# Kernel tuning notes

Measured on AMD Instinct MI355X. Metric: run time of the kernel, lower is better.

Reference implementation:

```python
import jax, jax.numpy as jnp
import numpy as np

B, S, IN, OUT = 4, 2048, 4096, 1024
ROUNDS = 12  # prime_factors(4096) == [2]*12
QMIN, QMAX = -128, 127


def _create_noise(key, shape, lo, hi):
    # Obfuscation noise spanning the data range; exactly corrected in forward.
    return jax.random.uniform(key, shape, jnp.float32, -0.5, 0.5) * (hi - lo)


def setup_inputs() -> dict:
    key = jax.random.key(0)
    ks = jax.random.split(key, 6)
    x = jax.random.normal(ks[0], (B, S, IN), jnp.float32)
    weight = jax.random.normal(ks[1], (OUT, IN), jnp.float32) * 0.02
    bias = jax.random.normal(ks[2], (OUT,), jnp.float32) * 0.02
    weight_noise = _create_noise(ks[3], (OUT, IN), weight.min(), weight.max())
    noise_x = _create_noise(ks[4], (B, S, IN), x.min(), x.max())
    # one random permutation of in_features per round
    perms = jnp.stack([jax.random.permutation(jax.random.fold_in(key, 1000 + r), IN)
                       for r in range(ROUNDS)]).astype(jnp.int32)
    # 2048 random orthogonal 2x2 blocks per round (rotations, like ortho_group with dim=2)
    theta = jax.random.uniform(ks[5], (ROUNDS, IN // 2), jnp.float32, 0.0, 2.0 * np.pi)
    c, s = jnp.cos(theta), jnp.sin(theta)
    row0 = jnp.stack([c, -s], axis=-1)
    row1 = jnp.stack([s, c], axis=-1)
    matrices = jnp.stack([row0, row1], axis=-2)  # (ROUNDS, IN//2, 2, 2)
    return {"x": x, "weight": weight, "bias": bias, "weight_noise": weight_noise,
            "noise_x": noise_x, "permutations": perms, "matrices": matrices}


def _permute_matrix_operation(X, perms, mats):
    # X: (..., n, cols). Each round: gather rows by permutation, then apply a
    # block-diagonal orthogonal transform (G blocks of size f along the n axis).
    lead = X.shape[:-2]
    n, cols = X.shape[-2], X.shape[-1]
    G, f = mats.shape[1], mats.shape[2]
    for r in range(mats.shape[0]):
        X = jnp.take(X, perms[r], axis=-2)
        Xb = X.reshape(lead + (G, f, cols))
        X = jnp.einsum('gij,...gjc->...gic', mats[r], Xb).reshape(lead + (n, cols))
    return X


def _quant_dequant(t):
    # Asymmetric per-tensor quantize -> round -> clamp -> dequantize (int8-style).
    lo, hi = t.min(), t.max()
    scale = (hi - lo) / (QMAX - QMIN)
    zp = jnp.round(QMIN - lo / scale)
    q = jnp.clip(jnp.round(t / scale + zp), QMIN, QMAX)
    return (q - zp) * scale


def reference(x, weight, bias, weight_noise, noise_x, permutations, matrices):
    # inverse-transpose blocks; equals `matrices` for orthogonal blocks, kept explicit for fidelity
    inv_mats_mT = jnp.swapaxes(jnp.linalg.inv(matrices), -1, -2)
    w_plus = weight + weight_noise                                   # (OUT, IN)
    permuted_w = jnp.swapaxes(
        _permute_matrix_operation(jnp.swapaxes(w_plus, -1, -2), permutations, inv_mats_mT), -1, -2)
    qw = _quant_dequant(permuted_w)                                  # (OUT, IN)
    permuted_x = jnp.swapaxes(
        _permute_matrix_operation(jnp.swapaxes(x + noise_x, -1, -2), permutations, matrices), -1, -2)
    qx = _quant_dequant(permuted_x)                                  # (B, S, IN)
    res = qx @ qw.T + bias                                           # quantized matmul + bias
    res = res - x @ weight_noise.T                                   # correction term 1
    res = res - noise_x @ w_plus.T                                   # correction term 2
    return res
```

## Files before the change

kernel.cpp:

```cpp
#include <hip/hip_runtime.h>


#define IN_F   4096
#define OUT_F  1024
#define MROWS  8192
#define KTOT   12288
#define KHALF  6144
#define NPASS  6
#define NTIL   96

typedef _Float16 f16;
typedef _Float16 f16x8 __attribute__((ext_vector_type(8)));
typedef _Float16 f16x4 __attribute__((ext_vector_type(4)));
typedef float    f32x4 __attribute__((ext_vector_type(4)));

#define OFF_XT  (0ull)
#define OFF_WT  (OFF_XT + (size_t)MROWS * IN_F * 4)
#define OFF_A   (OFF_WT + (size_t)OUT_F * IN_F * 4)
#define OFF_B   (OFF_A + (size_t)MROWS * KTOT * 2)
#define OFF_MM  (OFF_B + (size_t)OUT_F * KTOT * 2)
#define OFF_TIX (OFF_MM + 256)
#define OFF_TCX (OFF_TIX + (size_t)NPASS * 2048 * 8)
#define OFF_TIW (OFF_TCX + (size_t)NPASS * 2048 * 32)
#define OFF_TCW (OFF_TIW + (size_t)NPASS * 2048 * 8)

#define SW(s) ((s) ^ (((s) >> 3) & 7))

__device__ __forceinline__ unsigned enc_f(float f) {
  unsigned u = __float_as_uint(f);
  return (u & 0x80000000u) ? ~u : (u | 0x80000000u);
}
__device__ __forceinline__ float dec_f(unsigned u) {
  unsigned b = (u & 0x80000000u) ? (u & 0x7fffffffu) : ~u;
  return __uint_as_float(b);
}

__device__ __forceinline__ float4 f4comb(float4 c, float4 x0, float4 x1,
                                         float4 x2, float4 x3) {
  return make_float4(c.x * x0.x + c.y * x1.x + c.z * x2.x + c.w * x3.x,
                     c.x * x0.y + c.y * x1.y + c.z * x2.y + c.w * x3.y,
                     c.x * x0.z + c.y * x1.z + c.z * x2.z + c.w * x3.z,
                     c.x * x0.w + c.y * x1.w + c.z * x2.w + c.w * x3.w);
}

__global__ __launch_bounds__(256) void build_tables_kernel(
    const int* __restrict__ perms, const float* __restrict__ mats,
    uint2* __restrict__ tIx, float4* __restrict__ tCx,
    uint2* __restrict__ tIw, float4* __restrict__ tCw,
    unsigned* __restrict__ mm) {
  if (blockIdx.x == 0 && threadIdx.x == 0) {
    mm[0] = 0xFFFFFFFFu; mm[1] = 0u; mm[2] = 0xFFFFFFFFu; mm[3] = 0u;
  }
  int p = blockIdx.x >> 3;
  int g = ((blockIdx.x & 7) << 8) + threadIdx.x;
  int r0 = 2 * p, r1 = 2 * p + 1;
  {
    int q0 = perms[r1 * IN_F + 2 * g], q1 = perms[r1 * IN_F + 2 * g + 1];
    int a0 = q0 >> 1, e0 = q0 & 1, a1 = q1 >> 1, e1 = q1 & 1;
    unsigned i0 = perms[r0 * IN_F + 2 * a0], i1 = perms[r0 * IN_F + 2 * a0 + 1];
    unsigned i2 = perms[r0 * IN_F + 2 * a1], i3 = perms[r0 * IN_F + 2 * a1 + 1];
    uint2 idx = make_uint2(i0 | (i1 << 16), i2 | (i3 << 16));
    const float* Ma = mats + ((size_t)r0 * 2048 + a0) * 4;
    const float* Mb = mats + ((size_t)r0 * 2048 + a1) * 4;
    const float* M1 = mats + ((size_t)r1 * 2048 + g) * 4;
    int o = p * 2048 + g;
    {
      float c00 = Ma[e0 * 2], c01 = Ma[e0 * 2 + 1];
      float c10 = Mb[e1 * 2], c11 = Mb[e1 * 2 + 1];
      float m00 = M1[0], m01 = M1[1], m10 = M1[2], m11 = M1[3];
      tIx[o] = idx;
      tCx[2 * o]     = make_float4(m00 * c00, m00 * c01, m01 * c10, m01 * c11);
      tCx[2 * o + 1] = make_float4(m10 * c00, m10 * c01, m11 * c10, m11 * c11);
    }
    {
      float rda = 1.0f / (Ma[0] * Ma[3] - Ma[1] * Ma[2]);
      float rdb = 1.0f / (Mb[0] * Mb[3] - Mb[1] * Mb[2]);
      float rd1 = 1.0f / (M1[0] * M1[3] - M1[1] * M1[2]);
      float c00 = (e0 == 0 ? Ma[3] : -Ma[1]) * rda;
      float c01 = (e0 == 0 ? -Ma[2] : Ma[0]) * rda;
      float c10 = (e1 == 0 ? Mb[3] : -Mb[1]) * rdb;
      float c11 = (e1 == 0 ? -Mb[2] : Mb[0]) * rdb;
      float m00 = M1[3] * rd1, m01 = -M1[2] * rd1;
      float m10 = -M1[1] * rd1, m11 = M1[0] * rd1;
      tIw[o] = idx;
      tCw[2 * o]     = make_float4(m00 * c00, m00 * c01, m01 * c10, m01 * c11);
      tCw[2 * o + 1] = make_float4(m10 * c00, m10 * c01, m11 * c10, m11 * c11);
    }
  }
}

__global__ __launch_bounds__(1024) void transform_kernel(
    const float* __restrict__ x, const float* __restrict__ nx,
    const float* __restrict__ w, const float* __restrict__ wn,
    const uint2* __restrict__ tIx, const float4* __restrict__ tCx,
    const uint2* __restrict__ tIw, const float4* __restrict__ tCw,
    float* __restrict__ xt, float* __restrict__ wt,
    f16* __restrict__ Aall, f16* __restrict__ Ball,
    unsigned* __restrict__ mm) {
  extern __shared__ float4 buf[];
  const int t = threadIdx.x;
  const bool isW = blockIdx.x >= (MROWS / 4);
  const float *in0, *in1; const uint2* tI; const float4* tC;
  float* tout; f16* fout; int mmidx; size_t m0;
  if (!isW) {
    m0 = (size_t)blockIdx.x * 4;
    in0 = x; in1 = nx; tI = tIx; tC = tCx; tout = xt; fout = Aall; mmidx = 0;
  } else {
    m0 = (size_t)(blockIdx.x - MROWS / 4) * 4;
    in0 = w; in1 = wn; tI = tIw; tC = tCw; tout = wt; fout = Ball; mmidx = 2;
  }

  {
    float4 a0 = ((const float4*)(in0 + (m0 + 0) * IN_F))[t];
    float4 a1 = ((const float4*)(in0 + (m0 + 1) * IN_F))[t];
    float4 a2 = ((const float4*)(in0 + (m0 + 2) * IN_F))[t];
    float4 a3 = ((const float4*)(in0 + (m0 + 3) * IN_F))[t];
    float4 b0 = ((const float4*)(in1 + (m0 + 0) * IN_F))[t];
    float4 b1 = ((const float4*)(in1 + (m0 + 1) * IN_F))[t];
    float4 b2 = ((const float4*)(in1 + (m0 + 2) * IN_F))[t];
    float4 b3 = ((const float4*)(in1 + (m0 + 3) * IN_F))[t];
    float4 s0 = make_float4(a0.x + b0.x, a0.y + b0.y, a0.z + b0.z, a0.w + b0.w);
    float4 s1 = make_float4(a1.x + b1.x, a1.y + b1.y, a1.z + b1.z, a1.w + b1.w);
    float4 s2 = make_float4(a2.x + b2.x, a2.y + b2.y, a2.z + b2.z, a2.w + b2.w);
    float4 s3 = make_float4(a3.x + b3.x, a3.y + b3.y, a3.z + b3.z, a3.w + b3.w);
    int c = t * 4;
    buf[SW(c + 0)] = make_float4(s0.x, s1.x, s2.x, s3.x);
    buf[SW(c + 1)] = make_float4(s0.y, s1.y, s2.y, s3.y);
    buf[SW(c + 2)] = make_float4(s0.z, s1.z, s2.z, s3.z);
    buf[SW(c + 3)] = make_float4(s0.w, s1.w, s2.w, s3.w);
#pragma unroll
    for (int r = 0; r < 4; r++) {
      float4 av = r == 0 ? a0 : r == 1 ? a1 : r == 2 ? a2 : a3;
      float4 bv = r == 0 ? b0 : r == 1 ? b1 : r == 2 ? b2 : b3;
      float4 sv = r == 0 ? s0 : r == 1 ? s1 : r == 2 ? s2 : s3;
      f16* fr = fout + (m0 + r) * KTOT;
      f16x4 p, q;
      if (isW) {
        p.x=(f16)bv.x; p.y=(f16)bv.y; p.z=(f16)bv.z; p.w=(f16)bv.w;
        q.x=(f16)sv.x; q.y=(f16)sv.y; q.z=(f16)sv.z; q.w=(f16)sv.w;
      } else {
        p.x=(f16)(-av.x); p.y=(f16)(-av.y); p.z=(f16)(-av.z); p.w=(f16)(-av.w);
        q.x=(f16)(-bv.x); q.y=(f16)(-bv.y); q.z=(f16)(-bv.z); q.w=(f16)(-bv.w);
      }
      *(f16x4*)(fr + IN_F + c)     = p;
      *(f16x4*)(fr + 2 * IN_F + c) = q;
    }
  }
  __syncthreads();

  int cur = 0;
  for (int pass = 0; pass < NPASS; pass++) {
    const uint2* ti = tI + pass * 2048;
    const float4* tc = tC + (size_t)pass * 4096;
    const float4* bc = buf + cur * 4096;
    float4* bn = buf + (cur ^ 1) * 4096;
#pragma unroll
    for (int i = 0; i < 2; i++) {
      int g = i * 1024 + t;
      uint2 pk = ti[g];
      float4 cA = tc[2 * g], cB = tc[2 * g + 1];
      float4 x0 = bc[SW(pk.x & 0xffff)], x1 = bc[SW(pk.x >> 16)];
      float4 x2 = bc[SW(pk.y & 0xffff)], x3 = bc[SW(pk.y >> 16)];
      bn[SW(2 * g)]     = f4comb(cA, x0, x1, x2, x3);
      bn[SW(2 * g + 1)] = f4comb(cB, x0, x1, x2, x3);
    }
    cur ^= 1;
    __syncthreads();
  }
  float lmin = 3.4e38f, lmax = -3.4e38f;
  {
    int c = t * 4;
    float4 q0 = buf[SW(c + 0)];
    float4 q1 = buf[SW(c + 1)];
    float4 q2 = buf[SW(c + 2)];
    float4 q3 = buf[SW(c + 3)];
    ((float4*)(tout + (m0 + 0) * IN_F))[t] = make_float4(q0.x, q1.x, q2.x, q3.x);
    ((float4*)(tout + (m0 + 1) * IN_F))[t] = make_float4(q0.y, q1.y, q2.y, q3.y);
    ((float4*)(tout + (m0 + 2) * IN_F))[t] = make_float4(q0.z, q1.z, q2.z, q3.z);
    ((float4*)(tout + (m0 + 3) * IN_F))[t] = make_float4(q0.w, q1.w, q2.w, q3.w);
    float mn0 = fminf(fminf(q0.x, q0.y), fminf(q0.z, q0.w));
    float mn1 = fminf(fminf(q1.x, q1.y), fminf(q1.z, q1.w));
    float mn2 = fminf(fminf(q2.x, q2.y), fminf(q2.z, q2.w));
    float mn3 = fminf(fminf(q3.x, q3.y), fminf(q3.z, q3.w));
    float mx0 = fmaxf(fmaxf(q0.x, q0.y), fmaxf(q0.z, q0.w));
    float mx1 = fmaxf(fmaxf(q1.x, q1.y), fmaxf(q1.z, q1.w));
    float mx2 = fmaxf(fmaxf(q2.x, q2.y), fmaxf(q2.z, q2.w));
    float mx3 = fmaxf(fmaxf(q3.x, q3.y), fmaxf(q3.z, q3.w));
    lmin = fminf(fminf(mn0, mn1), fminf(mn2, mn3));
    lmax = fmaxf(fmaxf(mx0, mx1), fmaxf(mx2, mx3));
  }
#pragma unroll
  for (int off = 32; off > 0; off >>= 1) {
    lmin = fminf(lmin, __shfl_down(lmin, off));
    lmax = fmaxf(lmax, __shfl_down(lmax, off));
  }
  float* red = (float*)(buf + 4096);
  int wid = t >> 6;
  if ((t & 63) == 0) { red[wid * 2] = lmin; red[wid * 2 + 1] = lmax; }
  __syncthreads();
  if (t == 0) {
    float bmin = red[0], bmax = red[1];
#pragma unroll
    for (int i = 1; i < 16; i++) {
      bmin = fminf(bmin, red[i * 2]);
      bmax = fmaxf(bmax, red[i * 2 + 1]);
    }
    atomicMin(&mm[mmidx], enc_f(bmin));
    atomicMax(&mm[mmidx + 1], enc_f(bmax));
  }
}

__global__ void finalize_kernel(unsigned* mm) {
  float* sc = (float*)(mm + 4);
  float xlo = dec_f(mm[0]), xhi = dec_f(mm[1]);
  float wlo = dec_f(mm[2]), whi = dec_f(mm[3]);
  float sx = (xhi - xlo) / 255.0f;
  float zx = rintf(-128.0f - xlo / sx);
  float sw = (whi - wlo) / 255.0f;
  float zw = rintf(-128.0f - wlo / sw);
  sc[0] = sx; sc[1] = zx; sc[2] = sw; sc[3] = zw;
}

#define NQB ((MROWS + OUT_F) / 4)
__global__ __launch_bounds__(256) void quant_kernel(
    const float* __restrict__ xt, const float* __restrict__ wt,
    f16* __restrict__ Aall, f16* __restrict__ Ball,
    const unsigned* __restrict__ mm,
    const float* __restrict__ bias, float* __restrict__ out) {
  if (blockIdx.x >= NQB) {
    const float4* b4 = (const float4*)bias;
    float4* o4 = (float4*)out;
    int idx = (blockIdx.x - NQB) * 256 + threadIdx.x;
    const int total = MROWS * OUT_F / 4;
    for (int i = idx; i < total; i += 512 * 256)
      o4[i] = b4[i & (OUT_F / 4 - 1)];
    return;
  }
  const float* sc = (const float*)(mm + 4);
  const bool isW = blockIdx.x >= (MROWS / 4);
  size_t m0 = (size_t)(isW ? blockIdx.x - MROWS / 4 : blockIdx.x) * 4;
  float s = isW ? sc[2] : sc[0], zp = isW ? sc[3] : sc[1];
  int t = threadIdx.x;
#pragma unroll
  for (int r = 0; r < 4; r++) {
    const float4* srow = (const float4*)((isW ? wt : xt) + (m0 + r) * IN_F);
    f16* drow = (isW ? Ball : Aall) + (m0 + r) * KTOT;
#pragma unroll
    for (int j = 0; j < 4; j++) {
      int i4 = j * 256 + t;
      float4 v = srow[i4];
      float q0 = (fminf(fmaxf(rintf(v.x / s + zp), -128.f), 127.f) - zp) * s;
      float q1 = (fminf(fmaxf(rintf(v.y / s + zp), -128.f), 127.f) - zp) * s;
      float q2 = (fminf(fmaxf(rintf(v.z / s + zp), -128.f), 127.f) - zp) * s;
      float q3 = (fminf(fmaxf(rintf(v.w / s + zp), -128.f), 127.f) - zp) * s;
      f16x4 o; o.x = (f16)q0; o.y = (f16)q1; o.z = (f16)q2; o.w = (f16)q3;
      *(f16x4*)(drow + i4 * 4) = o;
    }
  }
}

__device__ __forceinline__ void gl2lds16(const void* g, void* l) {
  __builtin_amdgcn_global_load_lds(
      (__attribute__((address_space(1))) void*)g,
      (__attribute__((address_space(3))) void*)l, 16, 0, 0);
}

#define GBAR() asm volatile("s_barrier" ::: "memory")
#define MFMA16(d, va, vb) d = __builtin_amdgcn_mfma_f32_16x16x32_f16(va, vb, d, 0, 0, 0)

#define STAGE(t, hh) do {                                                   \
    const int c_ = (t) & 1;                                                 \
    if ((hh) < 2) {                                                         \
      const f16* g_ = gA + (size_t)((hh) * 128) * KTOT + (size_t)(t) * 64;  \
      f16* l_ = As + c_ * 16384 + (hh) * 8192 + sbase;                      \
      gl2lds16(g_, l_);                                                     \
      gl2lds16(g_ + (size_t)64 * KTOT, l_ + 4096);                          \
    } else {                                                                \
      const f16* g_ = gB + (size_t)(((hh) - 2) * 128) * KTOT + (size_t)(t) * 64; \
      f16* l_ = Bs + c_ * 16384 + ((hh) - 2) * 8192 + sbase;                \
      gl2lds16(g_, l_);                                                     \
      gl2lds16(g_ + (size_t)64 * KTOT, l_ + 4096);                          \
    }                                                                       \
  } while (0)

__global__ __launch_bounds__(512, 2) void gemm_kernel(
    const f16* __restrict__ A, const f16* __restrict__ B,
    float* __restrict__ out) {
  extern __shared__ f16 sm[];
  f16* As = sm;
  f16* Bs = sm + 32768;

  const int tid = threadIdx.x;
  const int wave = tid >> 6, lane = tid & 63;
  const int fr = lane & 15, quad = lane >> 4;
  const int wm = wave >> 2, wn = wave & 3;

  const int orig = blockIdx.x;
  const int wg = (orig & 7) * 32 + (orig >> 3);
  const int ks = wg >> 7;
  const int rem = wg & 127;
  const int bn = rem >> 5, bm = rem & 31;
  const size_t k0 = (size_t)ks * KHALF;

  const int srow = (wave << 3) + (lane >> 3);
  const int scol = (((lane & 7) ^ (lane >> 3)) << 3);
  const f16* gA = A + ((size_t)bm * 256 + srow) * KTOT + k0 + scol;
  const f16* gB = B + ((size_t)bn * 256 + srow) * KTOT + k0 + scol;
  const int sbase = wave << 9;

  const int co0 = ((quad ^ (fr & 7)) << 3);
  const int co1 = co0 ^ 32;
  const f16* rA0 = As + wm * 8192 + fr * 64 + co0;
  const f16* rA1 = As + wm * 8192 + fr * 64 + co1;
  const f16* rB0 = Bs + (wn >> 1) * 8192 + (wn & 1) * 4096 + fr * 64 + co0;
  const f16* rB1 = Bs + (wn >> 1) * 8192 + (wn & 1) * 4096 + fr * 64 + co1;

  f16x8 a0[4][2], a1[4][2], bF[4][2];
  f32x4 acc[8][4] = {};

  STAGE(0, 0); STAGE(0, 1); STAGE(0, 2); STAGE(0, 3);
  STAGE(1, 0); STAGE(1, 1);
  asm volatile("s_waitcnt vmcnt(4)" ::: "memory");
  GBAR();

  for (int t = 0; t < NTIL; ++t) {
    const int c = t & 1;
    const f16* pa0 = rA0 + c * 16384;
    const f16* pa1 = rA1 + c * 16384;
    const f16* pb0 = rB0 + c * 16384;
    const f16* pb1 = rB1 + c * 16384;

#pragma unroll
    for (int i = 0; i < 4; i++) {
      a0[i][0] = *(const f16x8*)(pa0 + i * 1024);
      a0[i][1] = *(const f16x8*)(pa1 + i * 1024);
    }
#pragma unroll
    for (int j = 0; j < 4; j++) {
      bF[j][0] = *(const f16x8*)(pb0 + j * 1024);
      bF[j][1] = *(const f16x8*)(pb1 + j * 1024);
    }
#pragma unroll
    for (int i = 0; i < 4; i++) {
      a1[i][0] = *(const f16x8*)(pa0 + (4 + i) * 1024);
      a1[i][1] = *(const f16x8*)(pa1 + (4 + i) * 1024);
    }
    if (t + 1 < NTIL) { STAGE(t + 1, 2); STAGE(t + 1, 3); }

    __builtin_amdgcn_s_setprio(1);
#pragma unroll
    for (int i = 0; i < 4; i++)
#pragma unroll
      for (int j = 0; j < 4; j++) {
        MFMA16(acc[i][j], a0[i][0], bF[j][0]);
        MFMA16(acc[i][j], a0[i][1], bF[j][1]);
      }
    __builtin_amdgcn_s_setprio(0);

    asm volatile("s_waitcnt lgkmcnt(0)" ::: "memory");
    GBAR();
    if (t + 2 < NTIL) { STAGE(t + 2, 0); STAGE(t + 2, 1); }

    __builtin_amdgcn_s_setprio(1);
#pragma unroll
    for (int i = 0; i < 4; i++)
#pragma unroll
      for (int j = 0; j < 4; j++) {
        MFMA16(acc[4 + i][j], a1[i][0], bF[j][0]);
        MFMA16(acc[4 + i][j], a1[i][1], bF[j][1]);
      }
    __builtin_amdgcn_s_setprio(0);

    if (t + 2 < NTIL) {
      asm volatile("s_waitcnt vmcnt(4)" ::: "memory");
    } else if (t + 1 < NTIL) {
      asm volatile("s_waitcnt vmcnt(0)" ::: "memory");
    }
    GBAR();
  }

  const size_t orow = (size_t)bm * 256 + wm * 128 + quad * 4;
  const int ocol = bn * 256 + wn * 64 + fr;
#pragma unroll
  for (int mi = 0; mi < 8; mi++)
#pragma unroll
    for (int ni = 0; ni < 4; ni++)
#pragma unroll
      for (int e = 0; e < 4; e++)
        unsafeAtomicAdd(&out[(orow + mi * 16 + e) * OUT_F + (ocol + ni * 16)],
                        acc[mi][ni][e]);
}

extern "C" void kernel_launch(void* const* d_in, const int* in_sizes, int n_in,
                              void* d_out, int out_size, void* d_ws, size_t ws_size,
                              hipStream_t stream) {
  const float* x     = (const float*)d_in[0];
  const float* w     = (const float*)d_in[1];
  const float* bias  = (const float*)d_in[2];
  const float* wn    = (const float*)d_in[3];
  const float* nx    = (const float*)d_in[4];
  const int*   perms = (const int*)d_in[5];
  const float* mats  = (const float*)d_in[6];
  float* out = (float*)d_out;

  char* ws = (char*)d_ws;
  float* xt   = (float*)(ws + OFF_XT);
  float* wt   = (float*)(ws + OFF_WT);
  f16*   Aall = (f16*)(ws + OFF_A);
  f16*   Ball = (f16*)(ws + OFF_B);
  unsigned* mm = (unsigned*)(ws + OFF_MM);
  uint2*  tIx = (uint2*)(ws + OFF_TIX);
  float4* tCx = (float4*)(ws + OFF_TCX);
  uint2*  tIw = (uint2*)(ws + OFF_TIW);
  float4* tCw = (float4*)(ws + OFF_TCW);

  static int attr_set = 0;
  if (!attr_set) {
    (void)hipFuncSetAttribute(reinterpret_cast<const void*>(gemm_kernel),
                              hipFuncAttributeMaxDynamicSharedMemorySize, 131072);
    (void)hipFuncSetAttribute(reinterpret_cast<const void*>(transform_kernel),
                              hipFuncAttributeMaxDynamicSharedMemorySize, 131072);
    attr_set = 1;
  }

  build_tables_kernel<<<48, 256, 0, stream>>>(perms, mats, tIx, tCx, tIw, tCw, mm);
  transform_kernel<<<MROWS / 4 + OUT_F / 4, 1024, 131072, stream>>>(
      x, nx, w, wn, tIx, tCx, tIw, tCw, xt, wt, Aall, Ball, mm);
  finalize_kernel<<<1, 1, 0, stream>>>(mm);
  quant_kernel<<<NQB + 512, 256, 0, stream>>>(xt, wt, Aall, Ball, mm, bias, out);
  gemm_kernel<<<2 * (MROWS / 256) * (OUT_F / 256), 512, 131072, stream>>>(Aall, Ball, out);
}
```

Baseline: 661.5 us.

## Load B fragments directly from global into registers, stage only A in LDS

The GEMM no longer stages the B tile through shared memory. Each wave loads its B MFMA fragments straight from global memory into registers each k-step, while A keeps its double-buffered global-to-LDS path. This halves the LDS footprint to 64KB and removes one barrier per iteration. In exchange, B global loads sit on the critical path right before the MFMAs, the old deeper A prefetch is gone, and each iteration now waits with vmcnt(0), which can expose memory latency. B data is also re-fetched by both wave rows rather than shared.

Result: slower. 814.2 us (+23.1%).

```diff
diff --git a/kernel.cpp b/kernel.cpp
--- a/kernel.cpp
+++ b/kernel.cpp
@@ -268,19 +268,13 @@
 #define GBAR() asm volatile("s_barrier" ::: "memory")
 #define MFMA16(d, va, vb) d = __builtin_amdgcn_mfma_f32_16x16x32_f16(va, vb, d, 0, 0, 0)
 
-#define STAGE(t, hh) do {                                                   \
-    const int c_ = (t) & 1;                                                 \
-    if ((hh) < 2) {                                                         \
-      const f16* g_ = gA + (size_t)((hh) * 128) * KTOT + (size_t)(t) * 64;  \
-      f16* l_ = As + c_ * 16384 + (hh) * 8192 + sbase;                      \
-      gl2lds16(g_, l_);                                                     \
-      gl2lds16(g_ + (size_t)64 * KTOT, l_ + 4096);                          \
-    } else {                                                                \
-      const f16* g_ = gB + (size_t)(((hh) - 2) * 128) * KTOT + (size_t)(t) * 64; \
-      f16* l_ = Bs + c_ * 16384 + ((hh) - 2) * 8192 + sbase;                \
-      gl2lds16(g_, l_);                                                     \
-      gl2lds16(g_ + (size_t)64 * KTOT, l_ + 4096);                          \
-    }                                                                       \
+#define STAGEA(t) do {                                                      \
+    f16* l_ = As + ((t) & 1) * 16384 + sbase;                               \
+    const f16* g_ = gA + (size_t)(t) * 64;                                  \
+    gl2lds16(g_, l_);                                                       \
+    gl2lds16(g_ + (size_t)64 * KTOT,  l_ + 4096);                           \
+    gl2lds16(g_ + (size_t)128 * KTOT, l_ + 8192);                           \
+    gl2lds16(g_ + (size_t)192 * KTOT, l_ + 12288);                          \
   } while (0)
 
 __global__ __launch_bounds__(512, 2) void gemm_kernel(
@@ -288,7 +282,6 @@
     float* __restrict__ out) {
   extern __shared__ f16 sm[];
   f16* As = sm;
-  f16* Bs = sm + 32768;
 
   const int tid = threadIdx.x;
   const int wave = tid >> 6, lane = tid & 63;
@@ -305,30 +298,43 @@
   const int srow = (wave << 3) + (lane >> 3);
   const int scol = (((lane & 7) ^ (lane >> 3)) << 3);
   const f16* gA = A + ((size_t)bm * 256 + srow) * KTOT + k0 + scol;
-  const f16* gB = B + ((size_t)bn * 256 + srow) * KTOT + k0 + scol;
   const int sbase = wave << 9;
 
   const int co0 = ((quad ^ (fr & 7)) << 3);
   const int co1 = co0 ^ 32;
   const f16* rA0 = As + wm * 8192 + fr * 64 + co0;
   const f16* rA1 = As + wm * 8192 + fr * 64 + co1;
-  const f16* rB0 = Bs + (wn >> 1) * 8192 + (wn & 1) * 4096 + fr * 64 + co0;
-  const f16* rB1 = Bs + (wn >> 1) * 8192 + (wn & 1) * 4096 + fr * 64 + co1;
+
+  const f16* gB0 = B + ((size_t)(bn * 256 + wn * 64 + fr)) * KTOT + k0 + quad * 8;
+  const f16* gB1 = gB0 + (size_t)16 * KTOT;
+  const f16* gB2 = gB0 + (size_t)32 * KTOT;
+  const f16* gB3 = gB0 + (size_t)48 * KTOT;
 
   f16x8 a0[4][2], a1[4][2], bF[4][2];
   f32x4 acc[8][4] = {};
 
-  STAGE(0, 0); STAGE(0, 1); STAGE(0, 2); STAGE(0, 3);
-  STAGE(1, 0); STAGE(1, 1);
-  asm volatile("s_waitcnt vmcnt(4)" ::: "memory");
+  STAGEA(0);
+  asm volatile("s_waitcnt vmcnt(0)" ::: "memory");
   GBAR();
 
   for (int t = 0; t < NTIL; ++t) {
     const int c = t & 1;
     const f16* pa0 = rA0 + c * 16384;
     const f16* pa1 = rA1 + c * 16384;
-    const f16* pb0 = rB0 + c * 16384;
-    const f16* pb1 = rB1 + c * 16384;
+
+    if (t + 1 < NTIL) STAGEA(t + 1);
+
+    {
+      const size_t ko = (size_t)t * 64;
+      bF[0][0] = *(const f16x8*)(gB0 + ko);
+      bF[0][1] = *(const f16x8*)(gB0 + ko + 32);
+      bF[1][0] = *(const f16x8*)(gB1 + ko);
+      bF[1][1] = *(const f16x8*)(gB1 + ko + 32);
+      bF[2][0] = *(const f16x8*)(gB2 + ko);
+      bF[2][1] = *(const f16x8*)(gB2 + ko + 32);
+      bF[3][0] = *(const f16x8*)(gB3 + ko);
+      bF[3][1] = *(const f16x8*)(gB3 + ko + 32);
+    }
 
 #pragma unroll
     for (int i = 0; i < 4; i++) {
@@ -336,16 +342,10 @@
       a0[i][1] = *(const f16x8*)(pa1 + i * 1024);
     }
 #pragma unroll
-    for (int j = 0; j < 4; j++) {
-      bF[j][0] = *(const f16x8*)(pb0 + j * 1024);
-      bF[j][1] = *(const f16x8*)(pb1 + j * 1024);
-    }
-#pragma unroll
     for (int i = 0; i < 4; i++) {
       a1[i][0] = *(const f16x8*)(pa0 + (4 + i) * 1024);
       a1[i][1] = *(const f16x8*)(pa1 + (4 + i) * 1024);
     }
-    if (t + 1 < NTIL) { STAGE(t + 1, 2); STAGE(t + 1, 3); }
 
     __builtin_amdgcn_s_setprio(1);
 #pragma unroll
@@ -355,13 +355,6 @@
         MFMA16(acc[i][j], a0[i][0], bF[j][0]);
         MFMA16(acc[i][j], a0[i][1], bF[j][1]);
       }
-    __builtin_amdgcn_s_setprio(0);
-
-    asm volatile("s_waitcnt lgkmcnt(0)" ::: "memory");
-    GBAR();
-    if (t + 2 < NTIL) { STAGE(t + 2, 0); STAGE(t + 2, 1); }
-
-    __builtin_amdgcn_s_setprio(1);
 #pragma unroll
     for (int i = 0; i < 4; i++)
 #pragma unroll
@@ -371,11 +364,7 @@
       }
     __builtin_amdgcn_s_setprio(0);
 
-    if (t + 2 < NTIL) {
-      asm volatile("s_waitcnt vmcnt(4)" ::: "memory");
-    } else if (t + 1 < NTIL) {
-      asm volatile("s_waitcnt vmcnt(0)" ::: "memory");
-    }
+    asm volatile("s_waitcnt vmcnt(0) lgkmcnt(0)" ::: "memory");
     GBAR();
   }
 
@@ -428,5 +417,5 @@
       x, nx, w, wn, tIx, tCx, tIw, tCw, xt, wt, Aall, Ball, mm);
   finalize_kernel<<<1, 1, 0, stream>>>(mm);
   quant_kernel<<<NQB + 512, 256, 0, stream>>>(xt, wt, Aall, Ball, mm, bias, out);
-  gemm_kernel<<<2 * (MROWS / 256) * (OUT_F / 256), 512, 131072, stream>>>(Aall, Ball, out);
-}
+  gemm_kernel<<<2 * (MROWS / 256) * (OUT_F / 256), 512, 65536, stream>>>(Aall, Ball, out);
+}
```
